# Kernel tuning notes

Measured on AMD Instinct MI355X. Metric: run time of the kernel, lower is better.

The kernel has to match this reference:

```python
import jax, jax.numpy as jnp
import numpy as np

D_MODEL = 1024
IDX_DIM = 64
SEQ = 4096
D_STATE = 64
EXPAND = 1
HEADDIM = 32
D_CONV = 4
D_INNER = EXPAND * D_MODEL
NHEADS = D_INNER // HEADDIM
CONV_DIM = D_INNER + 2 * D_STATE
D_IN_PROJ = 2 * D_INNER + 2 * D_STATE + NHEADS  # z, xBC, dt


def setup_inputs() -> dict:
    key = jax.random.key(0)
    ks = jax.random.split(key, 8)
    def rn(k, shape, scale=1.0):
        return jax.random.normal(k, shape, jnp.float32) * scale
    return {
        "x": rn(ks[0], (SEQ, D_MODEL)),
        "W_in": rn(ks[1], (D_IN_PROJ, D_MODEL), D_MODEL ** -0.5),
        "conv_w": rn(ks[2], (CONV_DIM, D_CONV), D_CONV ** -0.5),
        "conv_b": jnp.zeros((CONV_DIM,), jnp.float32),
        "dt_bias": rn(ks[3], (NHEADS,)),
        "A_log": jnp.log(jnp.arange(1, NHEADS + 1, dtype=jnp.float32)),
        "D": jnp.ones((NHEADS,), jnp.float32),
        "norm_w": jnp.ones((D_INNER,), jnp.float32),
        "W_out": rn(ks[4], (D_MODEL, D_INNER), D_INNER ** -0.5),
        "W_q": rn(ks[5], (IDX_DIM, D_MODEL), D_MODEL ** -0.5),
        "W_k": rn(ks[6], (IDX_DIM, D_MODEL), D_MODEL ** -0.5),
    }


def _silu(v):
    return v * jax.nn.sigmoid(v)


def _mamba2(x, W_in, conv_w, conv_b, dt_bias, A_log, Dp, norm_w, W_out):
    L = x.shape[0]
    zxbcdt = x @ W_in.T  # [L, D_IN_PROJ]
    z, xBC, dt = jnp.split(zxbcdt, [D_INNER, D_INNER + CONV_DIM], axis=-1)
    # depthwise causal conv1d, kernel D_CONV
    xc = jax.lax.conv_general_dilated(
        xBC.T[None],               # [1, C, L]
        conv_w[:, None, :],        # [C, 1, K]
        (1,), [(D_CONV - 1, 0)], feature_group_count=CONV_DIM)[0].T
    xBC = _silu(xc + conv_b)
    xs, B, C = jnp.split(xBC, [D_INNER, D_INNER + D_STATE], axis=-1)
    xs = xs.reshape(L, NHEADS, HEADDIM)
    dt = jax.nn.softplus(dt + dt_bias)   # [L, H]
    A = -jnp.exp(A_log)                  # [H]

    def step(h, inp):
        x_t, B_t, C_t, dt_t = inp        # [H,P], [N], [N], [H]
        dA = jnp.exp(dt_t * A)           # [H]
        h = h * dA[:, None, None] + (dt_t[:, None] * x_t)[:, :, None] * B_t[None, None, :]
        return h, jnp.einsum('hpn,n->hp', h, C_t)

    h0 = jnp.zeros((NHEADS, HEADDIM, D_STATE), x.dtype)
    _, ys = jax.lax.scan(step, h0, (xs, B, C, dt))  # ys: [L, H, P]
    y = ys + Dp[None, :, None] * xs
    y = y.reshape(L, D_INNER)
    y = y * _silu(z)                                 # gated RMSNorm
    y = y * jax.lax.rsqrt(jnp.mean(y * y, axis=-1, keepdims=True) + 1e-5) * norm_w
    return y @ W_out.T


def reference(x, W_in, conv_w, conv_b, dt_bias, A_log, D, norm_w, W_out, W_q, W_k):
    L = x.shape[0]
    x_mamba = _mamba2(x, W_in, conv_w, conv_b, dt_bias, A_log, D, norm_w, W_out)
    q = x_mamba @ W_q.T                  # [L, IDX_DIM]
    k = x @ W_k.T                        # [L, IDX_DIM]
    scores = jnp.einsum('ti,si->ts', q, k) * (IDX_DIM ** -0.5)
    mask = jnp.tril(jnp.ones((L, L), dtype=bool))
    return jnp.where(mask, scores, -jnp.inf)
```

## Files before the change

kernel.cpp:

```cpp
#include <hip/hip_runtime.h>
#include <math.h>

#define L_SEQ 4096
#define DMODEL 1024
#define DINNER 1024
#define DSTATE 64
#define NH 32
#define HD 32
#define CONVD 1152
#define DPROJ2 2272
#define KOFF 2208
#define QC 128
#define NC 32

#define NEG_FILL (-1e30f)

typedef __attribute__((ext_vector_type(8))) short short8;
typedef __attribute__((ext_vector_type(4))) float f32x4;
typedef unsigned short u16;

__device__ __forceinline__ u16 f2bf(float f) {
  unsigned int u = __float_as_uint(f);
  unsigned int r = (u + 0x7fffu + ((u >> 16) & 1u)) >> 16;
  return (u16)r;
}
__device__ __forceinline__ float bf2f(u16 b) {
  unsigned int u = ((unsigned int)b) << 16;
  return __uint_as_float(u);
}
__device__ __forceinline__ short8 pack8(float4 a, float4 b) {
  short8 v;
  v[0] = (short)f2bf(a.x); v[1] = (short)f2bf(a.y);
  v[2] = (short)f2bf(a.z); v[3] = (short)f2bf(a.w);
  v[4] = (short)f2bf(b.x); v[5] = (short)f2bf(b.y);
  v[6] = (short)f2bf(b.z); v[7] = (short)f2bf(b.w);
  return v;
}

__device__ __forceinline__ void g2l16(const void* g, void* l) {
  __builtin_amdgcn_global_load_lds(
      (const __attribute__((address_space(1))) unsigned int*)g,
      (__attribute__((address_space(3))) unsigned int*)l, 16, 0, 0);
}

__global__ __launch_bounds__(256) void cast_bf16_k(const float* __restrict__ in,
                                                   u16* __restrict__ out, int n) {
  int i = (blockIdx.x * 256 + threadIdx.x) * 8;
  if (i >= n) return;
  float4 f0 = *(const float4*)(in + i);
  float4 f1 = *(const float4*)(in + i + 4);
  *(short8*)(out + i) = pack8(f0, f1);
}

__global__ __launch_bounds__(256) void gemm_bf16(const u16* __restrict__ A,
                                                 const u16* __restrict__ B,
                                                 u16* __restrict__ Cbf,
                                                 int M, int N, int K) {
  __shared__ u16 As[128 * 32];
  __shared__ u16 Bs[128 * 32];
  const int tid = threadIdx.x;
  const int wave = tid >> 6, lane = tid & 63;
  const int m0 = blockIdx.y * 128, n0 = blockIdx.x * 128;
  const int wm = (wave >> 1) * 64, wn = (wave & 1) * 64;
  const int l15 = lane & 15, quad = lane >> 4;

  const int c0 = tid, c1 = 256 + tid;
  const int r0 = c0 >> 2, q0 = (c0 & 3) ^ ((r0 >> 1) & 3);
  const int r1 = c1 >> 2, q1 = (c1 & 3) ^ ((r1 >> 1) & 3);
  const u16* a0 = A + (size_t)(m0 + r0) * K + q0 * 8;
  const u16* a1 = A + (size_t)(m0 + r1) * K + q1 * 8;
  const int bn0 = min(n0 + r0, N - 1), bn1 = min(n0 + r1, N - 1);
  const u16* b0 = B + (size_t)bn0 * K + q0 * 8;
  const u16* b1 = B + (size_t)bn1 * K + q1 * 8;
  char* ldsA0 = (char*)As + wave * 1024;
  char* ldsA1 = (char*)As + 4096 + wave * 1024;
  char* ldsB0 = (char*)Bs + wave * 1024;
  char* ldsB1 = (char*)Bs + 4096 + wave * 1024;

  int offA[4], offB[4];
#pragma unroll
  for (int i = 0; i < 4; i++) {
    int ra = wm + i * 16 + l15;
    offA[i] = ra * 32 + (quad ^ ((ra >> 1) & 3)) * 8;
    int rb = wn + i * 16 + l15;
    offB[i] = rb * 32 + (quad ^ ((rb >> 1) & 3)) * 8;
  }

  f32x4 acc[4][4] = {};
  for (int k0 = 0; k0 < K; k0 += 32) {
    g2l16(a0 + k0, ldsA0);
    g2l16(a1 + k0, ldsA1);
    g2l16(b0 + k0, ldsB0);
    g2l16(b1 + k0, ldsB1);
    __builtin_amdgcn_s_waitcnt(0);
    __syncthreads();
    short8 af[4], bf[4];
#pragma unroll
    for (int i = 0; i < 4; i++) af[i] = *(const short8*)(As + offA[i]);
#pragma unroll
    for (int i = 0; i < 4; i++) bf[i] = *(const short8*)(Bs + offB[i]);
#pragma unroll
    for (int mi = 0; mi < 4; mi++)
#pragma unroll
      for (int ni = 0; ni < 4; ni++)
        acc[mi][ni] = __builtin_amdgcn_mfma_f32_16x16x32_bf16(af[mi], bf[ni],
                                                              acc[mi][ni], 0, 0, 0);
    __syncthreads();
  }
#pragma unroll
  for (int mi = 0; mi < 4; mi++)
#pragma unroll
    for (int r = 0; r < 4; r++) {
      int grow = m0 + wm + mi * 16 + quad * 4 + r;
#pragma unroll
      for (int ni = 0; ni < 4; ni++) {
        int gcol = n0 + wn + ni * 16 + l15;
        if (gcol < N) Cbf[(size_t)grow * N + gcol] = f2bf(acc[mi][ni][r]);
      }
    }
}

__global__ __launch_bounds__(256) void gemm_n64(const u16* __restrict__ A,
                                                const u16* __restrict__ B,
                                                u16* __restrict__ Cbf,
                                                int M, int N, int K) {
  __shared__ u16 As[128 * 32];
  __shared__ u16 Bs[64 * 32];
  const int tid = threadIdx.x;
  const int wave = tid >> 6, lane = tid & 63;
  const int m0 = blockIdx.x * 128, n0 = blockIdx.y * 64;
  const int wm = (wave >> 1) * 64, wn = (wave & 1) * 32;
  const int l15 = lane & 15, quad = lane >> 4;

  const int c0 = tid, c1 = 256 + tid;
  const int r0 = c0 >> 2, q0 = (c0 & 3) ^ ((r0 >> 1) & 3);
  const int r1 = c1 >> 2, q1 = (c1 & 3) ^ ((r1 >> 1) & 3);
  const int rb = tid >> 2, qb = (tid & 3) ^ ((rb >> 1) & 3);
  const u16* a0 = A + (size_t)(m0 + r0) * K + q0 * 8;
  const u16* a1 = A + (size_t)(m0 + r1) * K + q1 * 8;
  const u16* bptr = B + (size_t)(n0 + rb) * K + qb * 8;
  char* ldsA0 = (char*)As + wave * 1024;
  char* ldsA1 = (char*)As + 4096 + wave * 1024;
  char* ldsB = (char*)Bs + wave * 1024;

  int offA[4], offB[2];
#pragma unroll
  for (int i = 0; i < 4; i++) {
    int ra = wm + i * 16 + l15;
    offA[i] = ra * 32 + (quad ^ ((ra >> 1) & 3)) * 8;
  }
#pragma unroll
  for (int j = 0; j < 2; j++) {
    int rr = wn + j * 16 + l15;
    offB[j] = rr * 32 + (quad ^ ((rr >> 1) & 3)) * 8;
  }

  f32x4 acc[4][2] = {};
  for (int k0 = 0; k0 < K; k0 += 32) {
    g2l16(a0 + k0, ldsA0);
    g2l16(a1 + k0, ldsA1);
    g2l16(bptr + k0, ldsB);
    __builtin_amdgcn_s_waitcnt(0);
    __syncthreads();
    short8 af[4], bfr[2];
#pragma unroll
    for (int i = 0; i < 4; i++) af[i] = *(const short8*)(As + offA[i]);
#pragma unroll
    for (int j = 0; j < 2; j++) bfr[j] = *(const short8*)(Bs + offB[j]);
#pragma unroll
    for (int mi = 0; mi < 4; mi++)
#pragma unroll
      for (int ni = 0; ni < 2; ni++)
        acc[mi][ni] = __builtin_amdgcn_mfma_f32_16x16x32_bf16(af[mi], bfr[ni],
                                                              acc[mi][ni], 0, 0, 0);
    __syncthreads();
  }
#pragma unroll
  for (int mi = 0; mi < 4; mi++)
#pragma unroll
    for (int r = 0; r < 4; r++) {
      int grow = m0 + wm + mi * 16 + quad * 4 + r;
#pragma unroll
      for (int ni = 0; ni < 2; ni++)
        Cbf[(size_t)grow * N + n0 + wn + ni * 16 + l15] = f2bf(acc[mi][ni][r]);
    }
}

__global__ __launch_bounds__(256) void splitk64(const u16* __restrict__ A,
                                                const u16* __restrict__ B,
                                                float* __restrict__ P,
                                                int M, int K) {
  __shared__ u16 As[128 * 32];
  __shared__ u16 Bs[64 * 32];
  const int tid = threadIdx.x;
  const int wave = tid >> 6, lane = tid & 63;
  const int m0 = blockIdx.x * 128;
  const int ks = blockIdx.y;
  const int wm = (wave >> 1) * 64, wn = (wave & 1) * 32;
  const int l15 = lane & 15, quad = lane >> 4;

  const int c0 = tid, c1 = 256 + tid;
  const int r0 = c0 >> 2, q0 = (c0 & 3) ^ ((r0 >> 1) & 3);
  const int r1 = c1 >> 2, q1 = (c1 & 3) ^ ((r1 >> 1) & 3);
  const int rb = tid >> 2, qb = (tid & 3) ^ ((rb >> 1) & 3);
  const u16* a0 = A + (size_t)(m0 + r0) * K + q0 * 8;
  const u16* a1 = A + (size_t)(m0 + r1) * K + q1 * 8;
  const u16* bptr = B + (size_t)rb * K + qb * 8;
  char* ldsA0 = (char*)As + wave * 1024;
  char* ldsA1 = (char*)As + 4096 + wave * 1024;
  char* ldsB = (char*)Bs + wave * 1024;

  int offA[4], offB[2];
#pragma unroll
  for (int i = 0; i < 4; i++) {
    int ra = wm + i * 16 + l15;
    offA[i] = ra * 32 + (quad ^ ((ra >> 1) & 3)) * 8;
  }
#pragma unroll
  for (int j = 0; j < 2; j++) {
    int rr = wn + j * 16 + l15;
    offB[j] = rr * 32 + (quad ^ ((rr >> 1) & 3)) * 8;
  }

  f32x4 acc[4][2] = {};
  const int kbeg = ks * 128;
  for (int k0 = kbeg; k0 < kbeg + 128; k0 += 32) {
    g2l16(a0 + k0, ldsA0);
    g2l16(a1 + k0, ldsA1);
    g2l16(bptr + k0, ldsB);
    __builtin_amdgcn_s_waitcnt(0);
    __syncthreads();
    short8 af[4], bfr[2];
#pragma unroll
    for (int i = 0; i < 4; i++) af[i] = *(const short8*)(As + offA[i]);
#pragma unroll
    for (int j = 0; j < 2; j++) bfr[j] = *(const short8*)(Bs + offB[j]);
#pragma unroll
    for (int mi = 0; mi < 4; mi++)
#pragma unroll
      for (int ni = 0; ni < 2; ni++)
        acc[mi][ni] = __builtin_amdgcn_mfma_f32_16x16x32_bf16(af[mi], bfr[ni],
                                                              acc[mi][ni], 0, 0, 0);
    __syncthreads();
  }
  float* Pp = P + (size_t)ks * M * 64;
#pragma unroll
  for (int mi = 0; mi < 4; mi++)
#pragma unroll
    for (int r = 0; r < 4; r++) {
      int grow = m0 + wm + mi * 16 + quad * 4 + r;
#pragma unroll
      for (int ni = 0; ni < 2; ni++)
        Pp[(size_t)grow * 64 + wn + ni * 16 + l15] = acc[mi][ni][r];
    }
}

__global__ __launch_bounds__(256) void reduce8_k(const float* __restrict__ P,
                                                 u16* __restrict__ out, int n) {
  int i = blockIdx.x * 256 + threadIdx.x;
  if (i >= n) return;
  float s = 0.f;
#pragma unroll
  for (int ks = 0; ks < 8; ks++) s += P[(size_t)ks * n + i];
  out[i] = f2bf(s);
}

__global__ __launch_bounds__(256) void conv_silu_k(const u16* __restrict__ zx,
                                                   const float* __restrict__ cw,
                                                   const float* __restrict__ cb,
                                                   u16* __restrict__ xbc) {
  int c0 = threadIdx.x * 8;
  int t = blockIdx.x;
  if (c0 >= CONVD) return;
  float acc[8];
#pragma unroll
  for (int j = 0; j < 8; j++) acc[j] = cb[c0 + j];
  float wv[8][4];
#pragma unroll
  for (int j = 0; j < 8; j++) {
    float4 w4 = *(const float4*)(cw + (c0 + j) * 4);
    wv[j][0] = w4.x; wv[j][1] = w4.y; wv[j][2] = w4.z; wv[j][3] = w4.w;
  }
#pragma unroll
  for (int k = 0; k < 4; k++) {
    int s = t - 3 + k;
    if (s >= 0) {
      short8 v = *(const short8*)(zx + (size_t)s * DPROJ2 + DINNER + c0);
#pragma unroll
      for (int j = 0; j < 8; j++) acc[j] += bf2f((u16)v[j]) * wv[j][k];
    }
  }
  short8 o;
#pragma unroll
  for (int j = 0; j < 8; j++) o[j] = (short)f2bf(acc[j] / (1.f + expf(-acc[j])));
  *(short8*)(xbc + (size_t)t * CONVD + c0) = o;
}

__global__ void dtcum_k(const u16* __restrict__ zx,
                        const float* __restrict__ dt_bias,
                        const float* __restrict__ A_log,
                        float* __restrict__ dtsp,
                        float* __restrict__ aL) {
  int h = blockIdx.x & 31, c = blockIdx.x >> 5;
  int lane = threadIdx.x;
  float negA = -expf(A_log[h]);
  float bias = dt_bias[h];
  float carry = 0.f;
#pragma unroll
  for (int seg = 0; seg < 2; seg++) {
    int t = c * QC + seg * 64 + lane;
    float xv = bf2f(zx[(size_t)t * DPROJ2 + 2176 + h]) + bias;
    float sp = (xv > 20.f) ? xv : log1pf(expf(xv));
    dtsp[(size_t)t * 32 + h] = sp;
    float v = sp * negA;
#pragma unroll
    for (int off = 1; off < 64; off <<= 1) {
      float u = __shfl_up(v, off, 64);
      if (lane >= off) v += u;
    }
    aL[(size_t)t * 32 + h] = carry + v;
    carry += __shfl(v, 63, 64);
  }
}

__global__ __launch_bounds__(256) void chunk_state_mfma(const u16* __restrict__ xbc,
                                                        const float* __restrict__ dtsp,
                                                        const float* __restrict__ aL,
                                                        float* __restrict__ S) {
  int h = blockIdx.x & 31, c = blockIdx.x >> 5;
  int tid = threadIdx.x;
  __shared__ __align__(16) u16 sXs[32 * 136];
  __shared__ __align__(16) u16 sBT[64 * 136];
  __shared__ float scoef[QC];
  if (tid < QC) {
    float aend = aL[(size_t)(c * QC + QC - 1) * 32 + h];
    float a = aL[(size_t)(c * QC + tid) * 32 + h];
    scoef[tid] = expf(aend - a) * dtsp[(size_t)(c * QC + tid) * 32 + h];
  }
  __syncthreads();
  for (int j = tid; j < 32 * QC / 8; j += 256) {
    int s = j & 127, p0 = (j >> 7) * 8;
    short8 v = *(const short8*)(xbc + (size_t)(c * QC + s) * CONVD + h * HD + p0);
    float cf = scoef[s];
#pragma unroll
    for (int e = 0; e < 8; e++) sXs[(p0 + e) * 136 + s] = f2bf(cf * bf2f((u16)v[e]));
  }
  for (int j = tid; j < 64 * QC / 8; j += 256) {
    int s = j & 127, n0 = (j >> 7) * 8;
    short8 v = *(const short8*)(xbc + (size_t)(c * QC + s) * CONVD + DINNER + n0);
#pragma unroll
    for (int e = 0; e < 8; e++) sBT[(n0 + e) * 136 + s] = (u16)v[e];
  }
  __syncthreads();
  const int wave = tid >> 6, lane = tid & 63;
  const int l15 = lane & 15, quad = lane >> 4;
  f32x4 acc[2] = {};
#pragma unroll
  for (int kk = 0; kk < 4; kk++) {
    short8 b = *(const short8*)(sBT + (wave * 16 + l15) * 136 + kk * 32 + quad * 8);
#pragma unroll
    for (int i = 0; i < 2; i++) {
      short8 a = *(const short8*)(sXs + (i * 16 + l15) * 136 + kk * 32 + quad * 8);
      acc[i] = __builtin_amdgcn_mfma_f32_16x16x32_bf16(a, b, acc[i], 0, 0, 0);
    }
  }
  float* Sb = S + ((size_t)c * 32 + h) * 2048;
#pragma unroll
  for (int i = 0; i < 2; i++)
#pragma unroll
    for (int r = 0; r < 4; r++) {
      int p = i * 16 + quad * 4 + r;
      Sb[p * 64 + wave * 16 + l15] = acc[i][r];
    }
}

__global__ __launch_bounds__(256) void state_scan_k(const float* __restrict__ S,
                                                    const float* __restrict__ aL,
                                                    float* __restrict__ Hinit) {
  int idx = blockIdx.x * 256 + threadIdx.x;
  int h = idx >> 11, rem = idx & 2047;
  float E = 0.f;
  for (int c = 0; c < NC; c++) {
    size_t o = ((size_t)c * 32 + h) * 2048 + rem;
    Hinit[o] = E;
    float dec = expf(aL[(size_t)(c * QC + QC - 1) * 32 + h]);
    E = E * dec + S[o];
  }
}

__global__ __launch_bounds__(256) void gmat_mfma(const u16* __restrict__ xbc,
                                                 float* __restrict__ G) {
  int c = blockIdx.x;
  int tid = threadIdx.x;
  const int wave = tid >> 6, lane = tid & 63;
  const int wm = (wave >> 1) * 64, wn = (wave & 1) * 64;
  const int l15 = lane & 15, quad = lane >> 4;
  f32x4 acc[4][4] = {};
#pragma unroll
  for (int kk = 0; kk < 2; kk++) {
    short8 a[4], b[4];
#pragma unroll
    for (int i = 0; i < 4; i++) {
      int t = wm + i * 16 + l15;
      a[i] = *(const short8*)(xbc + (size_t)(c * QC + t) * CONVD + DINNER + DSTATE + kk * 32 + quad * 8);
      int s = wn + i * 16 + l15;
      b[i] = *(const short8*)(xbc + (size_t)(c * QC + s) * CONVD + DINNER + kk * 32 + quad * 8);
    }
#pragma unroll
    for (int mi = 0; mi < 4; mi++)
#pragma unroll
      for (int ni = 0; ni < 4; ni++)
        acc[mi][ni] = __builtin_amdgcn_mfma_f32_16x16x32_bf16(a[mi], b[ni],
                                                              acc[mi][ni], 0, 0, 0);
  }
  float* Gb = G + (size_t)c * QC * QC;
#pragma unroll
  for (int mi = 0; mi < 4; mi++)
#pragma unroll
    for (int r = 0; r < 4; r++) {
      int t = wm + mi * 16 + quad * 4 + r;
#pragma unroll
      for (int ni = 0; ni < 4; ni++)
        Gb[(size_t)t * QC + wn + ni * 16 + l15] = acc[mi][ni][r];
    }
}

__global__ __launch_bounds__(256) void yout_mfma(const u16* __restrict__ xbc,
                                                 const float* __restrict__ dtsp,
                                                 const float* __restrict__ aL,
                                                 const float* __restrict__ G,
                                                 const float* __restrict__ Hinit,
                                                 const float* __restrict__ Dv,
                                                 u16* __restrict__ y) {
  int h = blockIdx.x & 31, c = blockIdx.x >> 5;
  int tid = threadIdx.x;
  __shared__ __align__(16) u16 sXT[32 * 136];
  __shared__ float sa[QC];
  __shared__ float sd[QC];

  if (tid < QC) {
    sa[tid] = aL[(size_t)(c * QC + tid) * 32 + h];
    sd[tid] = dtsp[(size_t)(c * QC + tid) * 32 + h];
  }
  for (int j = tid; j < 32 * QC / 8; j += 256) {
    int t = j & 127, p0 = (j >> 7) * 8;
    short8 v = *(const short8*)(xbc + (size_t)(c * QC + t) * CONVD + h * HD + p0);
#pragma unroll
    for (int e = 0; e < 8; e++) sXT[(p0 + e) * 136 + t] = (u16)v[e];
  }
  __syncthreads();

  const int wave = tid >> 6, lane = tid & 63;
  const int l15 = lane & 15, quad = lane >> 4;
  f32x4 acc1[2][2] = {};
  f32x4 acc2[2][2] = {};

#pragma unroll
  for (int kk = 0; kk < 4; kk++) {
    short8 b[2];
#pragma unroll
    for (int j = 0; j < 2; j++)
      b[j] = *(const short8*)(sXT + (j * 16 + l15) * 136 + kk * 32 + quad * 8);
#pragma unroll
    for (int i = 0; i < 2; i++) {
      int rmax = wave * 32 + i * 16 + 15;
      if (kk * 32 > rmax) continue;
      int m = wave * 32 + i * 16 + l15;
      float am = sa[m];
      const float* Gp = G + (size_t)c * QC * QC + (size_t)m * QC + kk * 32 + quad * 8;
      float4 g0 = *(const float4*)Gp;
      float4 g1 = *(const float4*)(Gp + 4);
      float gv[8] = {g0.x, g0.y, g0.z, g0.w, g1.x, g1.y, g1.z, g1.w};
      int s0 = kk * 32 + quad * 8;
      short8 a;
#pragma unroll
      for (int j2 = 0; j2 < 8; j2++) {
        int s = s0 + j2;
        float w = 0.f;
        if (s <= m) w = expf(am - sa[s]) * sd[s] * gv[j2];
        a[j2] = (short)f2bf(w);
      }
#pragma unroll
      for (int j = 0; j < 2; j++)
        acc1[i][j] = __builtin_amdgcn_mfma_f32_16x16x32_bf16(a, b[j], acc1[i][j], 0, 0, 0);
    }
  }

  const float* Hbase = Hinit + ((size_t)c * 32 + h) * 2048;
#pragma unroll
  for (int kk = 0; kk < 2; kk++) {
    short8 b[2];
#pragma unroll
    for (int j = 0; j < 2; j++) {
      const float* Hp = Hbase + (size_t)(j * 16 + l15) * 64 + kk * 32 + quad * 8;
      b[j] = pack8(*(const float4*)Hp, *(const float4*)(Hp + 4));
    }
#pragma unroll
    for (int i = 0; i < 2; i++) {
      int t = wave * 32 + i * 16 + l15;
      short8 a = *(const short8*)(xbc + (size_t)(c * QC + t) * CONVD + DINNER + DSTATE + kk * 32 + quad * 8);
#pragma unroll
      for (int j = 0; j < 2; j++)
        acc2[i][j] = __builtin_amdgcn_mfma_f32_16x16x32_bf16(a, b[j], acc2[i][j], 0, 0, 0);
    }
  }

  float Dh = Dv[h];
#pragma unroll
  for (int i = 0; i < 2; i++) {
#pragma unroll
    for (int r = 0; r < 4; r++) {
      int t = wave * 32 + i * 16 + quad * 4 + r;
      float et = expf(sa[t]);
#pragma unroll
      for (int j = 0; j < 2; j++) {
        int p = j * 16 + l15;
        float xv = bf2f(sXT[p * 136 + t]);
        float val = acc1[i][j][r] + et * acc2[i][j][r] + Dh * xv;
        y[(size_t)(c * QC + t) * DINNER + h * HD + p] = f2bf(val);
      }
    }
  }
}

__global__ __launch_bounds__(256) void rmsnorm_k(const u16* __restrict__ y1,
                                                 const u16* __restrict__ zx,
                                                 const float* __restrict__ nw,
                                                 u16* __restrict__ y2) {
  int t = blockIdx.x, tid = threadIdx.x;
  int d0 = tid * 4;
  ushort4 yv = *(const ushort4*)(y1 + (size_t)t * DINNER + d0);
  ushort4 zv = *(const ushort4*)(zx + (size_t)t * DPROJ2 + d0);
  float v[4];
  float ss = 0.f;
  u16 ya[4] = {yv.x, yv.y, yv.z, yv.w};
  u16 za[4] = {zv.x, zv.y, zv.z, zv.w};
#pragma unroll
  for (int i = 0; i < 4; i++) {
    float z = bf2f(za[i]);
    float val = bf2f(ya[i]) * (z / (1.f + expf(-z)));
    v[i] = val;
    ss += val * val;
  }
#pragma unroll
  for (int off = 32; off > 0; off >>= 1) ss += __shfl_xor(ss, off, 64);
  __shared__ float red[4];
  int wid = tid >> 6, lane = tid & 63;
  if (lane == 0) red[wid] = ss;
  __syncthreads();
  ss = red[0] + red[1] + red[2] + red[3];
  float scale = rsqrtf(ss * (1.f / 1024.f) + 1e-5f);
  float4 w4 = *(const float4*)(nw + d0);
  float wa[4] = {w4.x, w4.y, w4.z, w4.w};
  ushort4 o;
  o.x = f2bf(v[0] * scale * wa[0]);
  o.y = f2bf(v[1] * scale * wa[1]);
  o.z = f2bf(v[2] * scale * wa[2]);
  o.w = f2bf(v[3] * scale * wa[3]);
  *(ushort4*)(y2 + (size_t)t * DINNER + d0) = o;
}

__global__ __launch_bounds__(256) void scores_mfma(const u16* __restrict__ q,
                                                   const u16* __restrict__ kmat,
                                                   int kstride,
                                                   float* __restrict__ out) {
  const int m0 = blockIdx.y * 128, n0 = blockIdx.x * 128;
  const int tid = threadIdx.x;
  if (n0 > m0 + 127) {
    float4 f = make_float4(NEG_FILL, NEG_FILL, NEG_FILL, NEG_FILL);
    for (int i = tid; i < 128 * 32; i += 256) {
      int row = i >> 5, c4 = (i & 31) << 2;
      *(float4*)(out + (size_t)(m0 + row) * L_SEQ + n0 + c4) = f;
    }
    return;
  }
  const int wave = tid >> 6, lane = tid & 63;
  const int wm = (wave >> 1) * 64, wn = (wave & 1) * 64;
  const int l15 = lane & 15, quad = lane >> 4;
  f32x4 acc[4][4] = {};
#pragma unroll
  for (int kk = 0; kk < 2; kk++) {
    short8 a[4], b[4];
#pragma unroll
    for (int i = 0; i < 4; i++) {
      a[i] = *(const short8*)(q + (size_t)(m0 + wm + i * 16 + l15) * 64 + kk * 32 + quad * 8);
      b[i] = *(const short8*)(kmat + (size_t)(n0 + wn + i * 16 + l15) * kstride + kk * 32 + quad * 8);
    }
#pragma unroll
    for (int mi = 0; mi < 4; mi++)
#pragma unroll
      for (int ni = 0; ni < 4; ni++)
        acc[mi][ni] = __builtin_amdgcn_mfma_f32_16x16x32_bf16(a[mi], b[ni],
                                                              acc[mi][ni], 0, 0, 0);
  }
#pragma unroll
  for (int mi = 0; mi < 4; mi++)
#pragma unroll
    for (int r = 0; r < 4; r++) {
      int row = m0 + wm + mi * 16 + quad * 4 + r;
#pragma unroll
      for (int ni = 0; ni < 4; ni++) {
        int col = n0 + wn + ni * 16 + l15;
        out[(size_t)row * L_SEQ + col] = (col <= row) ? acc[mi][ni][r] * 0.125f : NEG_FILL;
      }
    }
}

extern "C" void kernel_launch(void* const* d_in, const int* in_sizes, int n_in,
                              void* d_out, int out_size, void* d_ws, size_t ws_size,
                              hipStream_t stream) {
  const float* x       = (const float*)d_in[0];
  const float* W_in    = (const float*)d_in[1];
  const float* conv_w  = (const float*)d_in[2];
  const float* conv_b  = (const float*)d_in[3];
  const float* dt_bias = (const float*)d_in[4];
  const float* A_log   = (const float*)d_in[5];
  const float* Dv      = (const float*)d_in[6];
  const float* norm_w  = (const float*)d_in[7];
  const float* W_out   = (const float*)d_in[8];
  const float* W_q     = (const float*)d_in[9];
  const float* W_k     = (const float*)d_in[10];
  float* out = (float*)d_out;

  char* ws = (char*)d_ws;
  size_t off = 0;
  auto alloc = [&](size_t bytes) {
    void* p = (void*)(ws + off);
    off += (bytes + 255) & ~(size_t)255;
    return p;
  };
  u16* zx_bf   = (u16*)alloc((size_t)L_SEQ * DPROJ2 * 2);
  u16* xbc_bf  = (u16*)alloc((size_t)L_SEQ * CONVD * 2);
  float* dtsp  = (float*)alloc((size_t)L_SEQ * NH * 4);
  float* aL    = (float*)alloc((size_t)L_SEQ * NH * 4);
  float* S     = (float*)alloc((size_t)NC * NH * HD * DSTATE * 4);
  float* Hinit = (float*)alloc((size_t)NC * NH * HD * DSTATE * 4);
  float* G     = (float*)alloc((size_t)NC * QC * QC * 4);
  u16* y1_bf   = (u16*)alloc((size_t)L_SEQ * DINNER * 2);
  u16* y2_bf   = (u16*)alloc((size_t)L_SEQ * DINNER * 2);
  u16* x_bf    = (u16*)alloc((size_t)L_SEQ * DMODEL * 2);
  u16* Wcat_bf = (u16*)alloc((size_t)DPROJ2 * DMODEL * 2);
  u16* Wout_bf = (u16*)alloc((size_t)DMODEL * DINNER * 2);
  u16* Wq_bf   = (u16*)alloc((size_t)64 * DMODEL * 2);
  u16* xm_bf   = (u16*)alloc((size_t)L_SEQ * DMODEL * 2);
  u16* q_bf    = (u16*)alloc((size_t)L_SEQ * 64 * 2);
  float* Pq = S;

  cast_bf16_k<<<dim3(L_SEQ * DMODEL / 2048), 256, 0, stream>>>(x, x_bf, L_SEQ * DMODEL);
  cast_bf16_k<<<dim3(2208 * DMODEL / 2048), 256, 0, stream>>>(W_in, Wcat_bf, 2208 * DMODEL);
  cast_bf16_k<<<dim3(64 * DMODEL / 2048), 256, 0, stream>>>(W_k, Wcat_bf + (size_t)2208 * DMODEL, 64 * DMODEL);
  cast_bf16_k<<<dim3(DMODEL * DINNER / 2048), 256, 0, stream>>>(W_out, Wout_bf, DMODEL * DINNER);
  cast_bf16_k<<<dim3(64 * DMODEL / 2048), 256, 0, stream>>>(W_q, Wq_bf, 64 * DMODEL);
  gemm_bf16<<<dim3((DPROJ2 + 127) / 128, L_SEQ / 128), 256, 0, stream>>>(
      x_bf, Wcat_bf, zx_bf, L_SEQ, DPROJ2, DMODEL);
  conv_silu_k<<<dim3(L_SEQ), 256, 0, stream>>>(zx_bf, conv_w, conv_b, xbc_bf);
  dtcum_k<<<dim3(NC * NH), 64, 0, stream>>>(zx_bf, dt_bias, A_log, dtsp, aL);
  chunk_state_mfma<<<dim3(NC * NH), 256, 0, stream>>>(xbc_bf, dtsp, aL, S);
  state_scan_k<<<dim3(NH * HD * DSTATE / 256), 256, 0, stream>>>(S, aL, Hinit);
  gmat_mfma<<<dim3(NC), 256, 0, stream>>>(xbc_bf, G);
  yout_mfma<<<dim3(NC * NH), 256, 0, stream>>>(xbc_bf, dtsp, aL, G, Hinit, Dv, y1_bf);
  rmsnorm_k<<<dim3(L_SEQ), 256, 0, stream>>>(y1_bf, zx_bf, norm_w, y2_bf);
  gemm_n64<<<dim3(L_SEQ / 128, DMODEL / 64), 256, 0, stream>>>(
      y2_bf, Wout_bf, xm_bf, L_SEQ, DMODEL, DINNER);
  splitk64<<<dim3(L_SEQ / 128, 8), 256, 0, stream>>>(xm_bf, Wq_bf, Pq, L_SEQ, DMODEL);
  reduce8_k<<<dim3(L_SEQ * 64 / 256), 256, 0, stream>>>(Pq, q_bf, L_SEQ * 64);
  scores_mfma<<<dim3(32, 32), 256, 0, stream>>>(q_bf, zx_bf + KOFF, DPROJ2, out);
}
```

Baseline: 269.1 us.

## Fold W_out into W_q to skip the output projection GEMM

Since q = (y2 @ W_out^T) @ W_q^T, the change precomputes Wqo = W_q @ W_out (64x1024) with a transpose-cast kernel and a small MFMA kernel. The 4096x1024x1024 output-projection GEMM is dropped, and the split-K q projection reads y2 directly. The in_proj GEMM also moves from the 128x128 tile kernel to the 128x64 kernel, with N-bounds guards added. The fused weight is rounded to bf16, so the rounding order differs from the reference and numerics may shift slightly.

Result: faster. 262.8 us (-2.3%).

```diff
diff --git a/kernel.cpp b/kernel.cpp
--- a/kernel.cpp
+++ b/kernel.cpp
@@ -52,71 +52,46 @@
   *(short8*)(out + i) = pack8(f0, f1);
 }
 
-__global__ __launch_bounds__(256) void gemm_bf16(const u16* __restrict__ A,
-                                                 const u16* __restrict__ B,
-                                                 u16* __restrict__ Cbf,
-                                                 int M, int N, int K) {
-  __shared__ u16 As[128 * 32];
-  __shared__ u16 Bs[128 * 32];
+__global__ __launch_bounds__(256) void transpose_cast_k(const float* __restrict__ in,
+                                                        u16* __restrict__ out) {
+  __shared__ float tile[64][65];
+  int tx = threadIdx.x & 63, ty = threadIdx.x >> 6;
+  int bx = blockIdx.x, by = blockIdx.y;
+#pragma unroll
+  for (int k = 0; k < 16; k++) {
+    int r = ty + k * 4;
+    tile[r][tx] = in[(size_t)(by * 64 + r) * 1024 + bx * 64 + tx];
+  }
+  __syncthreads();
+#pragma unroll
+  for (int k = 0; k < 16; k++) {
+    int r = ty + k * 4;
+    out[(size_t)(bx * 64 + r) * 1024 + by * 64 + tx] = f2bf(tile[tx][r]);
+  }
+}
+
+__global__ __launch_bounds__(256) void wqo_k(const u16* __restrict__ Wq,
+                                             const u16* __restrict__ WoutT,
+                                             u16* __restrict__ Wqo) {
   const int tid = threadIdx.x;
   const int wave = tid >> 6, lane = tid & 63;
-  const int m0 = blockIdx.y * 128, n0 = blockIdx.x * 128;
-  const int wm = (wave >> 1) * 64, wn = (wave & 1) * 64;
   const int l15 = lane & 15, quad = lane >> 4;
-
-  const int c0 = tid, c1 = 256 + tid;
-  const int r0 = c0 >> 2, q0 = (c0 & 3) ^ ((r0 >> 1) & 3);
-  const int r1 = c1 >> 2, q1 = (c1 & 3) ^ ((r1 >> 1) & 3);
-  const u16* a0 = A + (size_t)(m0 + r0) * K + q0 * 8;
-  const u16* a1 = A + (size_t)(m0 + r1) * K + q1 * 8;
-  const int bn0 = min(n0 + r0, N - 1), bn1 = min(n0 + r1, N - 1);
-  const u16* b0 = B + (size_t)bn0 * K + q0 * 8;
-  const u16* b1 = B + (size_t)bn1 * K + q1 * 8;
-  char* ldsA0 = (char*)As + wave * 1024;
-  char* ldsA1 = (char*)As + 4096 + wave * 1024;
-  char* ldsB0 = (char*)Bs + wave * 1024;
-  char* ldsB1 = (char*)Bs + 4096 + wave * 1024;
-
-  int offA[4], offB[4];
-#pragma unroll
-  for (int i = 0; i < 4; i++) {
-    int ra = wm + i * 16 + l15;
-    offA[i] = ra * 32 + (quad ^ ((ra >> 1) & 3)) * 8;
-    int rb = wn + i * 16 + l15;
-    offB[i] = rb * 32 + (quad ^ ((rb >> 1) & 3)) * 8;
-  }
-
-  f32x4 acc[4][4] = {};
-  for (int k0 = 0; k0 < K; k0 += 32) {
-    g2l16(a0 + k0, ldsA0);
-    g2l16(a1 + k0, ldsA1);
-    g2l16(b0 + k0, ldsB0);
-    g2l16(b1 + k0, ldsB1);
-    __builtin_amdgcn_s_waitcnt(0);
-    __syncthreads();
-    short8 af[4], bf[4];
-#pragma unroll
-    for (int i = 0; i < 4; i++) af[i] = *(const short8*)(As + offA[i]);
-#pragma unroll
-    for (int i = 0; i < 4; i++) bf[i] = *(const short8*)(Bs + offB[i]);
-#pragma unroll
-    for (int mi = 0; mi < 4; mi++)
-#pragma unroll
-      for (int ni = 0; ni < 4; ni++)
-        acc[mi][ni] = __builtin_amdgcn_mfma_f32_16x16x32_bf16(af[mi], bf[ni],
-                                                              acc[mi][ni], 0, 0, 0);
-    __syncthreads();
+  const int j0 = blockIdx.x * 64;
+  f32x4 acc[4] = {};
+  for (int kk = 0; kk < 32; kk++) {
+    short8 b = *(const short8*)(WoutT + (size_t)(j0 + wave * 16 + l15) * 1024 + kk * 32 + quad * 8);
+#pragma unroll
+    for (int mi = 0; mi < 4; mi++) {
+      short8 a = *(const short8*)(Wq + (size_t)(mi * 16 + l15) * 1024 + kk * 32 + quad * 8);
+      acc[mi] = __builtin_amdgcn_mfma_f32_16x16x32_bf16(a, b, acc[mi], 0, 0, 0);
+    }
   }
 #pragma unroll
   for (int mi = 0; mi < 4; mi++)
 #pragma unroll
     for (int r = 0; r < 4; r++) {
-      int grow = m0 + wm + mi * 16 + quad * 4 + r;
-#pragma unroll
-      for (int ni = 0; ni < 4; ni++) {
-        int gcol = n0 + wn + ni * 16 + l15;
-        if (gcol < N) Cbf[(size_t)grow * N + gcol] = f2bf(acc[mi][ni][r]);
-      }
+      int i = mi * 16 + quad * 4 + r;
+      Wqo[(size_t)i * 1024 + j0 + wave * 16 + l15] = f2bf(acc[mi][r]);
     }
 }
 
@@ -138,7 +113,8 @@
   const int rb = tid >> 2, qb = (tid & 3) ^ ((rb >> 1) & 3);
   const u16* a0 = A + (size_t)(m0 + r0) * K + q0 * 8;
   const u16* a1 = A + (size_t)(m0 + r1) * K + q1 * 8;
-  const u16* bptr = B + (size_t)(n0 + rb) * K + qb * 8;
+  const int bn = min(n0 + rb, N - 1);
+  const u16* bptr = B + (size_t)bn * K + qb * 8;
   char* ldsA0 = (char*)As + wave * 1024;
   char* ldsA1 = (char*)As + 4096 + wave * 1024;
   char* ldsB = (char*)Bs + wave * 1024;
@@ -181,8 +157,10 @@
     for (int r = 0; r < 4; r++) {
       int grow = m0 + wm + mi * 16 + quad * 4 + r;
 #pragma unroll
-      for (int ni = 0; ni < 2; ni++)
-        Cbf[(size_t)grow * N + n0 + wn + ni * 16 + l15] = f2bf(acc[mi][ni][r]);
+      for (int ni = 0; ni < 2; ni++) {
+        int gcol = n0 + wn + ni * 16 + l15;
+        if (gcol < N) Cbf[(size_t)grow * N + gcol] = f2bf(acc[mi][ni][r]);
+      }
     }
 }
 
@@ -380,6 +358,7 @@
   int idx = blockIdx.x * 256 + threadIdx.x;
   int h = idx >> 11, rem = idx & 2047;
   float E = 0.f;
+#pragma unroll
   for (int c = 0; c < NC; c++) {
     size_t o = ((size_t)c * 32 + h) * 2048 + rem;
     Hinit[o] = E;
@@ -629,29 +608,30 @@
     off += (bytes + 255) & ~(size_t)255;
     return p;
   };
-  u16* zx_bf   = (u16*)alloc((size_t)L_SEQ * DPROJ2 * 2);
-  u16* xbc_bf  = (u16*)alloc((size_t)L_SEQ * CONVD * 2);
-  float* dtsp  = (float*)alloc((size_t)L_SEQ * NH * 4);
-  float* aL    = (float*)alloc((size_t)L_SEQ * NH * 4);
-  float* S     = (float*)alloc((size_t)NC * NH * HD * DSTATE * 4);
-  float* Hinit = (float*)alloc((size_t)NC * NH * HD * DSTATE * 4);
-  float* G     = (float*)alloc((size_t)NC * QC * QC * 4);
-  u16* y1_bf   = (u16*)alloc((size_t)L_SEQ * DINNER * 2);
-  u16* y2_bf   = (u16*)alloc((size_t)L_SEQ * DINNER * 2);
-  u16* x_bf    = (u16*)alloc((size_t)L_SEQ * DMODEL * 2);
-  u16* Wcat_bf = (u16*)alloc((size_t)DPROJ2 * DMODEL * 2);
-  u16* Wout_bf = (u16*)alloc((size_t)DMODEL * DINNER * 2);
-  u16* Wq_bf   = (u16*)alloc((size_t)64 * DMODEL * 2);
-  u16* xm_bf   = (u16*)alloc((size_t)L_SEQ * DMODEL * 2);
-  u16* q_bf    = (u16*)alloc((size_t)L_SEQ * 64 * 2);
+  u16* zx_bf    = (u16*)alloc((size_t)L_SEQ * DPROJ2 * 2);
+  u16* xbc_bf   = (u16*)alloc((size_t)L_SEQ * CONVD * 2);
+  float* dtsp   = (float*)alloc((size_t)L_SEQ * NH * 4);
+  float* aL     = (float*)alloc((size_t)L_SEQ * NH * 4);
+  float* S      = (float*)alloc((size_t)NC * NH * HD * DSTATE * 4);
+  float* Hinit  = (float*)alloc((size_t)NC * NH * HD * DSTATE * 4);
+  float* G      = (float*)alloc((size_t)NC * QC * QC * 4);
+  u16* y1_bf    = (u16*)alloc((size_t)L_SEQ * DINNER * 2);
+  u16* y2_bf    = (u16*)alloc((size_t)L_SEQ * DINNER * 2);
+  u16* x_bf     = (u16*)alloc((size_t)L_SEQ * DMODEL * 2);
+  u16* Wcat_bf  = (u16*)alloc((size_t)DPROJ2 * DMODEL * 2);
+  u16* WoutT_bf = (u16*)alloc((size_t)DMODEL * DINNER * 2);
+  u16* Wq_bf    = (u16*)alloc((size_t)64 * DMODEL * 2);
+  u16* Wqo_bf   = (u16*)alloc((size_t)64 * DINNER * 2);
+  u16* q_bf     = (u16*)alloc((size_t)L_SEQ * 64 * 2);
   float* Pq = S;
 
   cast_bf16_k<<<dim3(L_SEQ * DMODEL / 2048), 256, 0, stream>>>(x, x_bf, L_SEQ * DMODEL);
   cast_bf16_k<<<dim3(2208 * DMODEL / 2048), 256, 0, stream>>>(W_in, Wcat_bf, 2208 * DMODEL);
   cast_bf16_k<<<dim3(64 * DMODEL / 2048), 256, 0, stream>>>(W_k, Wcat_bf + (size_t)2208 * DMODEL, 64 * DMODEL);
-  cast_bf16_k<<<dim3(DMODEL * DINNER / 2048), 256, 0, stream>>>(W_out, Wout_bf, DMODEL * DINNER);
   cast_bf16_k<<<dim3(64 * DMODEL / 2048), 256, 0, stream>>>(W_q, Wq_bf, 64 * DMODEL);
-  gemm_bf16<<<dim3((DPROJ2 + 127) / 128, L_SEQ / 128), 256, 0, stream>>>(
+  transpose_cast_k<<<dim3(16, 16), 256, 0, stream>>>(W_out, WoutT_bf);
+  wqo_k<<<dim3(16), 256, 0, stream>>>(Wq_bf, WoutT_bf, Wqo_bf);
+  gemm_n64<<<dim3(L_SEQ / 128, (DPROJ2 + 63) / 64), 256, 0, stream>>>(
       x_bf, Wcat_bf, zx_bf, L_SEQ, DPROJ2, DMODEL);
   conv_silu_k<<<dim3(L_SEQ), 256, 0, stream>>>(zx_bf, conv_w, conv_b, xbc_bf);
   dtcum_k<<<dim3(NC * NH), 64, 0, stream>>>(zx_bf, dt_bias, A_log, dtsp, aL);
@@ -660,9 +640,7 @@
   gmat_mfma<<<dim3(NC), 256, 0, stream>>>(xbc_bf, G);
   yout_mfma<<<dim3(NC * NH), 256, 0, stream>>>(xbc_bf, dtsp, aL, G, Hinit, Dv, y1_bf);
   rmsnorm_k<<<dim3(L_SEQ), 256, 0, stream>>>(y1_bf, zx_bf, norm_w, y2_bf);
-  gemm_n64<<<dim3(L_SEQ / 128, DMODEL / 64), 256, 0, stream>>>(
-      y2_bf, Wout_bf, xm_bf, L_SEQ, DMODEL, DINNER);
-  splitk64<<<dim3(L_SEQ / 128, 8), 256, 0, stream>>>(xm_bf, Wq_bf, Pq, L_SEQ, DMODEL);
+  splitk64<<<dim3(L_SEQ / 128, 8), 256, 0, stream>>>(y2_bf, Wqo_bf, Pq, L_SEQ, DINNER);
   reduce8_k<<<dim3(L_SEQ * 64 / 256), 256, 0, stream>>>(Pq, q_bf, L_SEQ * 64);
   scores_mfma<<<dim3(32, 32), 256, 0, stream>>>(q_bf, zx_bf + KOFF, DPROJ2, out);
 }
```
